# Kernel optimization log

Measured on AMD Instinct MI355X. Metric: run time of the kernel, lower is better.

Reference implementation:

```python
import jax, jax.numpy as jnp
import numpy as np

N_NODES = 50000
N_EDGES = 800000


def gat_layer(x, src, dst, W, al, ar, b, activation):
    # x: [N, F_in], W: [F_in, H*D], al/ar: [H, D], b: [H*D]
    H, D = al.shape
    n = x.shape[0]
    h = (x @ W).reshape(n, H, D)                      # [N, H, D]
    el = jnp.sum(h * al, axis=-1)                     # [N, H]
    er = jnp.sum(h * ar, axis=-1)                     # [N, H]
    e = jax.nn.leaky_relu(el[src] + er[dst], 0.2)     # [E, H]
    # segment softmax over incoming edges of each dst node
    m = jax.ops.segment_max(e, dst, num_segments=n)   # [N, H]
    ex = jnp.exp(e - m[dst])                          # [E, H]
    s = jax.ops.segment_sum(ex, dst, num_segments=n)  # [N, H]
    a = ex / s[dst]                                   # [E, H]
    msg = h[src] * a[:, :, None]                      # [E, H, D]
    out = jax.ops.segment_sum(msg, dst, num_segments=n) + b.reshape(1, H, D)
    return activation(out) if activation is not None else out


def setup_inputs() -> dict:
    key = jax.random.key(0)
    ks = jax.random.split(key, 12)
    feat = jax.random.normal(ks[0], (N_NODES, 128), dtype=jnp.float32)
    src = jax.random.randint(ks[1], (N_EDGES,), 0, N_NODES)
    dst = jax.random.randint(ks[2], (N_EDGES,), 0, N_NODES)
    sc = 0.1
    return {
        "feat": feat, "src": src, "dst": dst,
        "W1": jax.random.normal(ks[3], (128, 256), jnp.float32) * sc,
        "al1": jax.random.normal(ks[4], (4, 64), jnp.float32) * sc,
        "ar1": jax.random.normal(ks[5], (4, 64), jnp.float32) * sc,
        "b1": jnp.zeros((256,), jnp.float32),
        "W2": jax.random.normal(ks[6], (256, 256), jnp.float32) * sc,
        "al2": jax.random.normal(ks[7], (4, 64), jnp.float32) * sc,
        "ar2": jax.random.normal(ks[8], (4, 64), jnp.float32) * sc,
        "b2": jnp.zeros((256,), jnp.float32),
        "W3": jax.random.normal(ks[9], (256, 8), jnp.float32) * sc,
        "al3": jax.random.normal(ks[10], (1, 8), jnp.float32) * sc,
        "ar3": jax.random.normal(ks[11], (1, 8), jnp.float32) * sc,
        "b3": jnp.zeros((8,), jnp.float32),
    }


def reference(feat, src, dst, W1, al1, ar1, b1, W2, al2, ar2, b2, W3, al3, ar3, b3):
    n = feat.shape[0]
    elu = jax.nn.elu
    h = gat_layer(feat, src, dst, W1, al1, ar1, b1, elu).reshape(n, -1)  # flatten heads
    h = gat_layer(h, src, dst, W2, al2, ar2, b2, elu).reshape(n, -1)
    h = gat_layer(h, src, dst, W3, al3, ar3, b3, None)                   # [N, 1, out]
    return h.mean(axis=1)                                               # head mean -> [N, out]
```

## Files before the change

kernel.cpp:

```cpp
#include <hip/hip_runtime.h>
#include <math.h>


typedef _Float16 half8 __attribute__((ext_vector_type(8)));
typedef _Float16 half4 __attribute__((ext_vector_type(4)));
typedef float    floatx4 __attribute__((ext_vector_type(4)));

#define SLOT_CAP 48

__device__ __forceinline__ float leaky02(float x) { return x > 0.f ? x : 0.2f * x; }

__global__ void build_prep(const int* __restrict__ src, const int* __restrict__ dst,
                           int* __restrict__ cnt, unsigned short* __restrict__ slots,
                           const float* __restrict__ W1, _Float16* __restrict__ W1T,
                           const float* __restrict__ W2, _Float16* __restrict__ W2T,
                           int E, int GE) {
    int b = blockIdx.x;
    if (b < GE) {
        int i = b * 256 + threadIdx.x;
        if (i < E) {
            int d = dst[i];
            int p = atomicAdd(&cnt[d], 1);
            if (p < SLOT_CAP) slots[d * SLOT_CAP + p] = (unsigned short)src[i];
        }
    } else {
        int i = (b - GE) * 256 + threadIdx.x;
        if (i < 128 * 256) {
            int m = i >> 7, k = i & 127;
            W1T[i] = (_Float16)W1[k * 256 + m];
        } else {
            int j = i - 128 * 256;
            if (j < 256 * 256) {
                int m = j >> 8, k = j & 255;
                W2T[j] = (_Float16)W2[k * 256 + m];
            }
        }
    }
}

#define GBM 128
#define GBK 32

template <bool AF32>
__global__ __launch_bounds__(256)
void gemm_mfma(const void* __restrict__ Ap, const _Float16* __restrict__ BT,
               _Float16* __restrict__ C, int N, int K) {
    __shared__ _Float16 As[GBM][GBK + 8];
    __shared__ _Float16 Bs[GBM][GBK + 8];
    int tid  = threadIdx.x;
    int wave = tid >> 6, lane = tid & 63;
    int quad = lane >> 4, l16 = lane & 15;
    int row0 = blockIdx.y * GBM;
    int col0 = blockIdx.x * GBM;

    floatx4 acc[8][2];
    #pragma unroll
    for (int i = 0; i < 8; ++i)
        #pragma unroll
        for (int j = 0; j < 2; ++j)
            #pragma unroll
            for (int e = 0; e < 4; ++e) acc[i][j][e] = 0.f;

    for (int k0 = 0; k0 < K; k0 += GBK) {
        if (AF32) {
            const float* Af = (const float*)Ap;
            #pragma unroll
            for (int it = 0; it < 4; ++it) {
                int s = it * 256 + tid;
                int r = s >> 3, off = (s & 7) * 4;
                float4 v = make_float4(0.f, 0.f, 0.f, 0.f);
                int gr = row0 + r;
                if (gr < N) v = *(const float4*)&Af[(size_t)gr * K + k0 + off];
                half4 hv;
                hv[0] = (_Float16)v.x; hv[1] = (_Float16)v.y;
                hv[2] = (_Float16)v.z; hv[3] = (_Float16)v.w;
                *(half4*)&As[r][off] = hv;
            }
        } else {
            const _Float16* Ah = (const _Float16*)Ap;
            #pragma unroll
            for (int it = 0; it < 2; ++it) {
                int s = it * 256 + tid;
                int r = s >> 2, off = (s & 3) * 8;
                half8 v;
                #pragma unroll
                for (int q = 0; q < 8; ++q) v[q] = (_Float16)0.f;
                int gr = row0 + r;
                if (gr < N) v = *(const half8*)&Ah[(size_t)gr * K + k0 + off];
                *(half8*)&As[r][off] = v;
            }
        }
        #pragma unroll
        for (int it = 0; it < 2; ++it) {
            int s = it * 256 + tid;
            int r = s >> 2, off = (s & 3) * 8;
            half8 w = *(const half8*)&BT[(size_t)(col0 + r) * K + k0 + off];
            *(half8*)&Bs[r][off] = w;
        }
        __syncthreads();
        half8 bfrag[2];
        #pragma unroll
        for (int ct = 0; ct < 2; ++ct)
            bfrag[ct] = *(const half8*)&Bs[wave * 32 + ct * 16 + l16][quad * 8];
        #pragma unroll
        for (int rt = 0; rt < 8; ++rt) {
            half8 afrag = *(const half8*)&As[rt * 16 + l16][quad * 8];
            acc[rt][0] = __builtin_amdgcn_mfma_f32_16x16x32_f16(afrag, bfrag[0], acc[rt][0], 0, 0, 0);
            acc[rt][1] = __builtin_amdgcn_mfma_f32_16x16x32_f16(afrag, bfrag[1], acc[rt][1], 0, 0, 0);
        }
        __syncthreads();
    }
    #pragma unroll
    for (int rt = 0; rt < 8; ++rt) {
        #pragma unroll
        for (int reg = 0; reg < 4; ++reg) {
            int gr = row0 + rt * 16 + quad * 4 + reg;
            if (gr < N) {
                #pragma unroll
                for (int ct = 0; ct < 2; ++ct) {
                    int gc = col0 + wave * 32 + ct * 16 + l16;
                    C[(size_t)gr * 256 + gc] = (_Float16)acc[rt][ct][reg];
                }
            }
        }
    }
}

__global__ __launch_bounds__(256)
void attn_lr(const _Float16* __restrict__ h16, const float* __restrict__ al,
             const float* __restrict__ ar, float* __restrict__ el,
             float* __restrict__ er, int NH) {
    int wid = (blockIdx.x * 256 + threadIdx.x) >> 6;
    int lane = threadIdx.x & 63;
    int r = lane >> 3, c = lane & 7;
    int row = wid * 8 + r;
    if (row >= NH) return;
    int hd = row & 3;
    half8 hv = *(const half8*)&h16[(size_t)row * 64 + c * 8];
    const float* alp = &al[hd * 64 + c * 8];
    const float* arp = &ar[hd * 64 + c * 8];
    float l = 0.f, rr = 0.f;
    #pragma unroll
    for (int q = 0; q < 8; ++q) {
        float v = (float)hv[q];
        l  += v * alp[q];
        rr += v * arp[q];
    }
    l  += __shfl_xor(l, 1);  l  += __shfl_xor(l, 2);  l  += __shfl_xor(l, 4);
    rr += __shfl_xor(rr, 1); rr += __shfl_xor(rr, 2); rr += __shfl_xor(rr, 4);
    if (c == 0) { el[row] = l; er[row] = rr; }
}

__global__ __launch_bounds__(256)
void gat_agg(const _Float16* __restrict__ h16, const float* __restrict__ el,
             const float* __restrict__ er, const int* __restrict__ cnt,
             const unsigned short* __restrict__ slots, const float* __restrict__ bias,
             _Float16* __restrict__ out, int N) {
    __shared__ int   sbuf[8][32];
    __shared__ float wbuf[8][32][4];
    int tid = threadIdx.x;
    int l32 = tid & 31;
    int g = tid >> 5;
    int node = blockIdx.x * 8 + g;
    if (node >= N) return;
    int deg = min(cnt[node], SLOT_CAP);
    int beg = node * SLOT_CAP, end = beg + deg;
    int hd = l32 >> 3;

    float4 ern4 = *(const float4*)&er[node * 4];
    float er0 = ern4.x, er1 = ern4.y, er2 = ern4.z, er3 = ern4.w;

    const _Float16* hb = h16 + l32 * 8;
    float acc[8] = {};

    if (deg <= 32) {
        bool act = l32 < deg;
        int sv = 0;
        float e0 = -INFINITY, e1 = -INFINITY, e2 = -INFINITY, e3 = -INFINITY;
        if (act) {
            sv = slots[beg + l32];
            float4 elv = *(const float4*)&el[sv * 4];
            e0 = leaky02(elv.x + er0);
            e1 = leaky02(elv.y + er1);
            e2 = leaky02(elv.z + er2);
            e3 = leaky02(elv.w + er3);
        }
        float m0 = e0, m1 = e1, m2 = e2, m3 = e3;
        #pragma unroll
        for (int msk = 1; msk < 32; msk <<= 1) {
            m0 = fmaxf(m0, __shfl_xor(m0, msk));
            m1 = fmaxf(m1, __shfl_xor(m1, msk));
            m2 = fmaxf(m2, __shfl_xor(m2, msk));
            m3 = fmaxf(m3, __shfl_xor(m3, msk));
        }
        float x0 = act ? __expf(e0 - m0) : 0.f;
        float x1 = act ? __expf(e1 - m1) : 0.f;
        float x2 = act ? __expf(e2 - m2) : 0.f;
        float x3 = act ? __expf(e3 - m3) : 0.f;
        float s0 = x0, s1 = x1, s2 = x2, s3 = x3;
        #pragma unroll
        for (int msk = 1; msk < 32; msk <<= 1) {
            s0 += __shfl_xor(s0, msk);
            s1 += __shfl_xor(s1, msk);
            s2 += __shfl_xor(s2, msk);
            s3 += __shfl_xor(s3, msk);
        }
        float i0 = s0 > 0.f ? 1.f / s0 : 0.f;
        float i1 = s1 > 0.f ? 1.f / s1 : 0.f;
        float i2 = s2 > 0.f ? 1.f / s2 : 0.f;
        float i3 = s3 > 0.f ? 1.f / s3 : 0.f;
        if (act) {
            sbuf[g][l32] = sv;
            wbuf[g][l32][0] = x0 * i0;
            wbuf[g][l32][1] = x1 * i1;
            wbuf[g][l32][2] = x2 * i2;
            wbuf[g][l32][3] = x3 * i3;
        }
        int t = 0;
        for (; t + 4 <= deg; t += 4) {
            int sa = sbuf[g][t],     sb = sbuf[g][t + 1];
            int sc = sbuf[g][t + 2], sd = sbuf[g][t + 3];
            float wa = wbuf[g][t][hd],     wb = wbuf[g][t + 1][hd];
            float wc = wbuf[g][t + 2][hd], wd = wbuf[g][t + 3][hd];
            half8 va = *(const half8*)&hb[(size_t)sa * 256];
            half8 vb = *(const half8*)&hb[(size_t)sb * 256];
            half8 vc = *(const half8*)&hb[(size_t)sc * 256];
            half8 vd = *(const half8*)&hb[(size_t)sd * 256];
            #pragma unroll
            for (int q = 0; q < 8; ++q)
                acc[q] += wa * (float)va[q] + wb * (float)vb[q]
                        + wc * (float)vc[q] + wd * (float)vd[q];
        }
        for (; t < deg; ++t) {
            int s = sbuf[g][t];
            float w = wbuf[g][t][hd];
            half8 v = *(const half8*)&hb[(size_t)s * 256];
            #pragma unroll
            for (int q = 0; q < 8; ++q) acc[q] += w * (float)v[q];
        }
    } else {
        float m0 = -INFINITY, m1 = -INFINITY, m2 = -INFINITY, m3 = -INFINITY;
        for (int j = beg + l32; j < end; j += 32) {
            int sv = slots[j];
            float4 elv = *(const float4*)&el[sv * 4];
            m0 = fmaxf(m0, leaky02(elv.x + er0));
            m1 = fmaxf(m1, leaky02(elv.y + er1));
            m2 = fmaxf(m2, leaky02(elv.z + er2));
            m3 = fmaxf(m3, leaky02(elv.w + er3));
        }
        #pragma unroll
        for (int msk = 1; msk < 32; msk <<= 1) {
            m0 = fmaxf(m0, __shfl_xor(m0, msk));
            m1 = fmaxf(m1, __shfl_xor(m1, msk));
            m2 = fmaxf(m2, __shfl_xor(m2, msk));
            m3 = fmaxf(m3, __shfl_xor(m3, msk));
        }
        float s0 = 0.f, s1 = 0.f, s2 = 0.f, s3 = 0.f;
        for (int j = beg + l32; j < end; j += 32) {
            int sv = slots[j];
            float4 elv = *(const float4*)&el[sv * 4];
            s0 += __expf(leaky02(elv.x + er0) - m0);
            s1 += __expf(leaky02(elv.y + er1) - m1);
            s2 += __expf(leaky02(elv.z + er2) - m2);
            s3 += __expf(leaky02(elv.w + er3) - m3);
        }
        #pragma unroll
        for (int msk = 1; msk < 32; msk <<= 1) {
            s0 += __shfl_xor(s0, msk);
            s1 += __shfl_xor(s1, msk);
            s2 += __shfl_xor(s2, msk);
            s3 += __shfl_xor(s3, msk);
        }
        float mh  = (hd & 2) ? ((hd & 1) ? m3 : m2) : ((hd & 1) ? m1 : m0);
        float sh_ = (hd & 2) ? ((hd & 1) ? s3 : s2) : ((hd & 1) ? s1 : s0);
        float erh = (hd & 2) ? ((hd & 1) ? er3 : er2) : ((hd & 1) ? er1 : er0);
        float ih  = sh_ > 0.f ? 1.f / sh_ : 0.f;
        int j = beg;
        for (; j + 4 <= end; j += 4) {
            int sa = slots[j], sb = slots[j + 1], sc = slots[j + 2], sd = slots[j + 3];
            float wa = __expf(leaky02(el[sa * 4 + hd] + erh) - mh) * ih;
            float wb = __expf(leaky02(el[sb * 4 + hd] + erh) - mh) * ih;
            float wc = __expf(leaky02(el[sc * 4 + hd] + erh) - mh) * ih;
            float wd = __expf(leaky02(el[sd * 4 + hd] + erh) - mh) * ih;
            half8 va = *(const half8*)&hb[(size_t)sa * 256];
            half8 vb = *(const half8*)&hb[(size_t)sb * 256];
            half8 vc = *(const half8*)&hb[(size_t)sc * 256];
            half8 vd = *(const half8*)&hb[(size_t)sd * 256];
            #pragma unroll
            for (int q = 0; q < 8; ++q)
                acc[q] += wa * (float)va[q] + wb * (float)vb[q]
                        + wc * (float)vc[q] + wd * (float)vd[q];
        }
        for (; j < end; ++j) {
            int sv = slots[j];
            float w = __expf(leaky02(el[sv * 4 + hd] + erh) - mh) * ih;
            half8 v = *(const half8*)&hb[(size_t)sv * 256];
            #pragma unroll
            for (int q = 0; q < 8; ++q) acc[q] += w * (float)v[q];
        }
    }

    half8 o;
    #pragma unroll
    for (int q = 0; q < 8; ++q) {
        float v = acc[q] + bias[l32 * 8 + q];
        v = v > 0.f ? v : (__expf(v) - 1.f);
        o[q] = (_Float16)v;
    }
    *(half8*)&out[(size_t)node * 256 + l32 * 8] = o;
}

__global__ __launch_bounds__(256)
void gemm3_attn(const _Float16* __restrict__ x, const float* __restrict__ W,
                const float* __restrict__ al, const float* __restrict__ ar,
                float* __restrict__ h3, float* __restrict__ el,
                float* __restrict__ er, int N) {
    int tid = threadIdx.x;
    int lane = tid & 63;
    int n = blockIdx.x * 4 + (tid >> 6);
    if (n >= N) return;
    float4 wr[8];
    const float4* Wp = (const float4*)&W[lane * 32];
    #pragma unroll
    for (int i = 0; i < 8; ++i) wr[i] = Wp[i];
    half4 xv = *(const half4*)&x[(size_t)n * 256 + lane * 4];
    float acc[8];
    #pragma unroll
    for (int d = 0; d < 8; ++d) acc[d] = 0.f;
    #pragma unroll
    for (int q = 0; q < 4; ++q) {
        float xq = (float)xv[q];
        float4 w0 = wr[q * 2], w1 = wr[q * 2 + 1];
        acc[0] += xq * w0.x; acc[1] += xq * w0.y;
        acc[2] += xq * w0.z; acc[3] += xq * w0.w;
        acc[4] += xq * w1.x; acc[5] += xq * w1.y;
        acc[6] += xq * w1.z; acc[7] += xq * w1.w;
    }
    #pragma unroll
    for (int d = 0; d < 8; ++d) {
        #pragma unroll
        for (int o = 32; o; o >>= 1) acc[d] += __shfl_down(acc[d], o);
    }
    if (lane == 0) {
        float l = 0.f, r = 0.f;
        #pragma unroll
        for (int d = 0; d < 8; ++d) {
            h3[n * 8 + d] = acc[d];
            l += acc[d] * al[d];
            r += acc[d] * ar[d];
        }
        el[n] = l;
        er[n] = r;
    }
}

__global__ __launch_bounds__(256)
void gat_agg3(const float* __restrict__ h3, const float* __restrict__ el,
              const float* __restrict__ er, const int* __restrict__ cnt,
              const unsigned short* __restrict__ slots, const float* __restrict__ bias,
              float* __restrict__ out, int N) {
    __shared__ int   sbuf3[4][64];
    __shared__ float wbuf3[4][64];
    int tid = threadIdx.x;
    int lane = tid & 63;
    int wv = tid >> 6;
    int n = blockIdx.x * 4 + wv;
    if (n >= N) return;
    int deg = min(cnt[n], SLOT_CAP);
    int beg = n * SLOT_CAP;
    float er_n = er[n];
    int g = lane >> 3, c = lane & 7;
    float acc = 0.f;
    bool act = lane < deg;
    int sv = 0;
    float e = -INFINITY;
    if (act) { sv = slots[beg + lane]; e = leaky02(el[sv] + er_n); }
    float mx = e;
    #pragma unroll
    for (int o = 1; o < 64; o <<= 1) mx = fmaxf(mx, __shfl_xor(mx, o));
    float ex = act ? __expf(e - mx) : 0.f;
    float sm = ex;
    #pragma unroll
    for (int o = 1; o < 64; o <<= 1) sm += __shfl_xor(sm, o);
    float inv = sm > 0.f ? 1.f / sm : 0.f;
    if (act) {
        sbuf3[wv][lane] = sv;
        wbuf3[wv][lane] = ex * inv;
    }
    for (int t = g; t < deg; t += 8) {
        int s = sbuf3[wv][t];
        float w = wbuf3[wv][t];
        acc += h3[s * 8 + c] * w;
    }
    acc += __shfl_xor(acc, 8);
    acc += __shfl_xor(acc, 16);
    acc += __shfl_xor(acc, 32);
    if (lane < 8) out[(size_t)n * 8 + lane] = acc + bias[lane];
}

static inline size_t align_up(size_t x, size_t a) { return (x + a - 1) & ~(a - 1); }

extern "C" void kernel_launch(void* const* d_in, const int* in_sizes, int n_in,
                              void* d_out, int out_size, void* d_ws, size_t ws_size,
                              hipStream_t stream) {
    const float* feat = (const float*)d_in[0];
    const int*   src  = (const int*)d_in[1];
    const int*   dst  = (const int*)d_in[2];
    const float* W1   = (const float*)d_in[3];
    const float* al1  = (const float*)d_in[4];
    const float* ar1  = (const float*)d_in[5];
    const float* b1   = (const float*)d_in[6];
    const float* W2   = (const float*)d_in[7];
    const float* al2  = (const float*)d_in[8];
    const float* ar2  = (const float*)d_in[9];
    const float* b2   = (const float*)d_in[10];
    const float* W3   = (const float*)d_in[11];
    const float* al3  = (const float*)d_in[12];
    const float* ar3  = (const float*)d_in[13];
    const float* b3   = (const float*)d_in[14];

    const int N = in_sizes[0] / 128;
    const int E = in_sizes[1];

    char* w = (char*)d_ws;
    _Float16* bufA16 = (_Float16*)w; w += align_up((size_t)N * 256 * 2, 256);
    _Float16* bufB16 = (_Float16*)w; w += align_up((size_t)N * 256 * 2, 256);
    _Float16* W1T    = (_Float16*)w; w += align_up((size_t)256 * 128 * 2, 256);
    _Float16* W2T    = (_Float16*)w; w += align_up((size_t)256 * 256 * 2, 256);
    float* el      = (float*)w; w += align_up((size_t)N * 4 * 4, 256);
    float* er      = (float*)w; w += align_up((size_t)N * 4 * 4, 256);
    int*   cnt     = (int*)w;   w += align_up((size_t)N * 4, 256);
    unsigned short* slots = (unsigned short*)w;
    w += align_up((size_t)N * SLOT_CAP * 2, 256);
    float* h3 = (float*)bufA16;
    (void)ws_size; (void)n_in; (void)out_size;

    const int GE = (E + 255) / 256;
    const int GT = (128 * 256 + 256 * 256 + 255) / 256;

    hipMemsetAsync(cnt, 0, (size_t)N * 4, stream);
    build_prep<<<GE + GT, 256, 0, stream>>>(src, dst, cnt, slots,
                                            W1, W1T, W2, W2T, E, GE);

    dim3 ggrid(2, (N + GBM - 1) / GBM);
    const int GA = (N + 7) / 8;
    const int GL = (N * 4 + 31) / 32;

    gemm_mfma<true><<<ggrid, 256, 0, stream>>>(feat, W1T, bufA16, N, 128);
    attn_lr<<<GL, 256, 0, stream>>>(bufA16, al1, ar1, el, er, N * 4);
    gat_agg<<<GA, 256, 0, stream>>>(bufA16, el, er, cnt, slots, b1, bufB16, N);

    gemm_mfma<false><<<ggrid, 256, 0, stream>>>(bufB16, W2T, bufA16, N, 256);
    attn_lr<<<GL, 256, 0, stream>>>(bufA16, al2, ar2, el, er, N * 4);
    gat_agg<<<GA, 256, 0, stream>>>(bufA16, el, er, cnt, slots, b2, bufB16, N);

    gemm3_attn<<<(N + 3) / 4, 256, 0, stream>>>(bufB16, W3, al3, ar3, h3, el, er, N);
    gat_agg3<<<(N + 3) / 4, 256, 0, stream>>>(h3, el, er, cnt, slots, b3,
                                              (float*)d_out, N);
}
```

Before: 390.8 us.

## Fuse all GAT stages into one persistent kernel with grid-wide barriers

Replaces the eight separate kernel launches with a single persistent kernel of 960 blocks. The blocks loop over virtual block indices for each stage and separate the stages with an atomic-counter grid barrier. The aim is to remove launch gaps and per-kernel tail effects. In exchange it depends on all 960 blocks being co-resident (four per CU is requested), otherwise the barrier deadlocks or hits its spin timeout. The barrier itself adds fence and spin cost, and the shared-memory footprint is now the GEMM's maximum for every stage.

```diff
diff --git a/kernel.cpp b/kernel.cpp
--- a/kernel.cpp
+++ b/kernel.cpp
@@ -7,51 +7,36 @@
 typedef float    floatx4 __attribute__((ext_vector_type(4)));
 
 #define SLOT_CAP 48
-
-__device__ __forceinline__ float leaky02(float x) { return x > 0.f ? x : 0.2f * x; }
-
-__global__ void build_prep(const int* __restrict__ src, const int* __restrict__ dst,
-                           int* __restrict__ cnt, unsigned short* __restrict__ slots,
-                           const float* __restrict__ W1, _Float16* __restrict__ W1T,
-                           const float* __restrict__ W2, _Float16* __restrict__ W2T,
-                           int E, int GE) {
-    int b = blockIdx.x;
-    if (b < GE) {
-        int i = b * 256 + threadIdx.x;
-        if (i < E) {
-            int d = dst[i];
-            int p = atomicAdd(&cnt[d], 1);
-            if (p < SLOT_CAP) slots[d * SLOT_CAP + p] = (unsigned short)src[i];
-        }
-    } else {
-        int i = (b - GE) * 256 + threadIdx.x;
-        if (i < 128 * 256) {
-            int m = i >> 7, k = i & 127;
-            W1T[i] = (_Float16)W1[k * 256 + m];
-        } else {
-            int j = i - 128 * 256;
-            if (j < 256 * 256) {
-                int m = j >> 8, k = j & 255;
-                W2T[j] = (_Float16)W2[k * 256 + m];
-            }
-        }
-    }
-}
-
 #define GBM 128
 #define GBK 32
+#define NBLK 960
+
+__device__ __forceinline__ float leaky02(float x) { return x > 0.f ? x : 0.2f * x; }
+
+__device__ __forceinline__ void gsync(int* bar, int target) {
+    __syncthreads();
+    if (threadIdx.x == 0) {
+        __threadfence();
+        atomicAdd(bar, 1);
+        int spins = 0;
+        while (__hip_atomic_load(bar, __ATOMIC_RELAXED, __HIP_MEMORY_SCOPE_AGENT) < target) {
+            if (++spins > (1 << 30)) break;
+        }
+        __threadfence();
+    }
+    __syncthreads();
+}
 
 template <bool AF32>
-__global__ __launch_bounds__(256)
-void gemm_mfma(const void* __restrict__ Ap, const _Float16* __restrict__ BT,
-               _Float16* __restrict__ C, int N, int K) {
-    __shared__ _Float16 As[GBM][GBK + 8];
-    __shared__ _Float16 Bs[GBM][GBK + 8];
+__device__ __forceinline__ void gemm_tile(char* smem, const void* __restrict__ Ap,
+                                          const _Float16* __restrict__ BT,
+                                          _Float16* __restrict__ C,
+                                          int row0, int col0, int N, int K) {
+    _Float16 (*As)[GBK + 8] = (_Float16 (*)[GBK + 8])smem;
+    _Float16 (*Bs)[GBK + 8] = (_Float16 (*)[GBK + 8])(smem + GBM * (GBK + 8) * 2);
     int tid  = threadIdx.x;
     int wave = tid >> 6, lane = tid & 63;
     int quad = lane >> 4, l16 = lane & 15;
-    int row0 = blockIdx.y * GBM;
-    int col0 = blockIdx.x * GBM;
 
     floatx4 acc[8][2];
     #pragma unroll
@@ -126,12 +111,13 @@
     }
 }
 
-__global__ __launch_bounds__(256)
-void attn_lr(const _Float16* __restrict__ h16, const float* __restrict__ al,
-             const float* __restrict__ ar, float* __restrict__ el,
-             float* __restrict__ er, int NH) {
-    int wid = (blockIdx.x * 256 + threadIdx.x) >> 6;
+__device__ __forceinline__ void attn_body(int vb, const _Float16* __restrict__ h16,
+                                          const float* __restrict__ al,
+                                          const float* __restrict__ ar,
+                                          float* __restrict__ el, float* __restrict__ er,
+                                          int NH) {
     int lane = threadIdx.x & 63;
+    int wid = vb * 4 + (threadIdx.x >> 6);
     int r = lane >> 3, c = lane & 7;
     int row = wid * 8 + r;
     if (row >= NH) return;
@@ -151,17 +137,20 @@
     if (c == 0) { el[row] = l; er[row] = rr; }
 }
 
-__global__ __launch_bounds__(256)
-void gat_agg(const _Float16* __restrict__ h16, const float* __restrict__ el,
-             const float* __restrict__ er, const int* __restrict__ cnt,
-             const unsigned short* __restrict__ slots, const float* __restrict__ bias,
-             _Float16* __restrict__ out, int N) {
-    __shared__ int   sbuf[8][32];
-    __shared__ float wbuf[8][32][4];
+__device__ __forceinline__ void agg_body(int vb, char* smem,
+                                         const _Float16* __restrict__ h16,
+                                         const float* __restrict__ el,
+                                         const float* __restrict__ er,
+                                         const int* __restrict__ cnt,
+                                         const unsigned short* __restrict__ slots,
+                                         const float* __restrict__ bias,
+                                         _Float16* __restrict__ out, int N) {
+    int (*sbuf)[32]     = (int (*)[32])smem;
+    float (*wbuf)[32][4] = (float (*)[32][4])(smem + 1024);
     int tid = threadIdx.x;
     int l32 = tid & 31;
     int g = tid >> 5;
-    int node = blockIdx.x * 8 + g;
+    int node = vb * 8 + g;
     if (node >= N) return;
     int deg = min(cnt[node], SLOT_CAP);
     int beg = node * SLOT_CAP, end = beg + deg;
@@ -223,12 +212,12 @@
             float wa = wbuf[g][t][hd],     wb = wbuf[g][t + 1][hd];
             float wc = wbuf[g][t + 2][hd], wd = wbuf[g][t + 3][hd];
             half8 va = *(const half8*)&hb[(size_t)sa * 256];
-            half8 vb = *(const half8*)&hb[(size_t)sb * 256];
+            half8 vb2 = *(const half8*)&hb[(size_t)sb * 256];
             half8 vc = *(const half8*)&hb[(size_t)sc * 256];
             half8 vd = *(const half8*)&hb[(size_t)sd * 256];
             #pragma unroll
             for (int q = 0; q < 8; ++q)
-                acc[q] += wa * (float)va[q] + wb * (float)vb[q]
+                acc[q] += wa * (float)va[q] + wb * (float)vb2[q]
                         + wc * (float)vc[q] + wd * (float)vd[q];
         }
         for (; t < deg; ++t) {
@@ -283,12 +272,12 @@
             float wc = __expf(leaky02(el[sc * 4 + hd] + erh) - mh) * ih;
             float wd = __expf(leaky02(el[sd * 4 + hd] + erh) - mh) * ih;
             half8 va = *(const half8*)&hb[(size_t)sa * 256];
-            half8 vb = *(const half8*)&hb[(size_t)sb * 256];
+            half8 vb2 = *(const half8*)&hb[(size_t)sb * 256];
             half8 vc = *(const half8*)&hb[(size_t)sc * 256];
             half8 vd = *(const half8*)&hb[(size_t)sd * 256];
             #pragma unroll
             for (int q = 0; q < 8; ++q)
-                acc[q] += wa * (float)va[q] + wb * (float)vb[q]
+                acc[q] += wa * (float)va[q] + wb * (float)vb2[q]
                         + wc * (float)vc[q] + wd * (float)vd[q];
         }
         for (; j < end; ++j) {
@@ -310,92 +299,165 @@
     *(half8*)&out[(size_t)node * 256 + l32 * 8] = o;
 }
 
-__global__ __launch_bounds__(256)
-void gemm3_attn(const _Float16* __restrict__ x, const float* __restrict__ W,
-                const float* __restrict__ al, const float* __restrict__ ar,
-                float* __restrict__ h3, float* __restrict__ el,
-                float* __restrict__ er, int N) {
-    int tid = threadIdx.x;
-    int lane = tid & 63;
-    int n = blockIdx.x * 4 + (tid >> 6);
-    if (n >= N) return;
-    float4 wr[8];
-    const float4* Wp = (const float4*)&W[lane * 32];
-    #pragma unroll
-    for (int i = 0; i < 8; ++i) wr[i] = Wp[i];
-    half4 xv = *(const half4*)&x[(size_t)n * 256 + lane * 4];
-    float acc[8];
-    #pragma unroll
-    for (int d = 0; d < 8; ++d) acc[d] = 0.f;
-    #pragma unroll
-    for (int q = 0; q < 4; ++q) {
-        float xq = (float)xv[q];
-        float4 w0 = wr[q * 2], w1 = wr[q * 2 + 1];
-        acc[0] += xq * w0.x; acc[1] += xq * w0.y;
-        acc[2] += xq * w0.z; acc[3] += xq * w0.w;
-        acc[4] += xq * w1.x; acc[5] += xq * w1.y;
-        acc[6] += xq * w1.z; acc[7] += xq * w1.w;
-    }
-    #pragma unroll
-    for (int d = 0; d < 8; ++d) {
-        #pragma unroll
-        for (int o = 32; o; o >>= 1) acc[d] += __shfl_down(acc[d], o);
-    }
-    if (lane == 0) {
-        float l = 0.f, r = 0.f;
-        #pragma unroll
-        for (int d = 0; d < 8; ++d) {
-            h3[n * 8 + d] = acc[d];
-            l += acc[d] * al[d];
-            r += acc[d] * ar[d];
-        }
-        el[n] = l;
-        er[n] = r;
-    }
-}
-
-__global__ __launch_bounds__(256)
-void gat_agg3(const float* __restrict__ h3, const float* __restrict__ el,
-              const float* __restrict__ er, const int* __restrict__ cnt,
-              const unsigned short* __restrict__ slots, const float* __restrict__ bias,
-              float* __restrict__ out, int N) {
-    __shared__ int   sbuf3[4][64];
-    __shared__ float wbuf3[4][64];
-    int tid = threadIdx.x;
-    int lane = tid & 63;
-    int wv = tid >> 6;
-    int n = blockIdx.x * 4 + wv;
-    if (n >= N) return;
-    int deg = min(cnt[n], SLOT_CAP);
-    int beg = n * SLOT_CAP;
-    float er_n = er[n];
-    int g = lane >> 3, c = lane & 7;
-    float acc = 0.f;
-    bool act = lane < deg;
-    int sv = 0;
-    float e = -INFINITY;
-    if (act) { sv = slots[beg + lane]; e = leaky02(el[sv] + er_n); }
-    float mx = e;
-    #pragma unroll
-    for (int o = 1; o < 64; o <<= 1) mx = fmaxf(mx, __shfl_xor(mx, o));
-    float ex = act ? __expf(e - mx) : 0.f;
-    float sm = ex;
-    #pragma unroll
-    for (int o = 1; o < 64; o <<= 1) sm += __shfl_xor(sm, o);
-    float inv = sm > 0.f ? 1.f / sm : 0.f;
-    if (act) {
-        sbuf3[wv][lane] = sv;
-        wbuf3[wv][lane] = ex * inv;
-    }
-    for (int t = g; t < deg; t += 8) {
-        int s = sbuf3[wv][t];
-        float w = wbuf3[wv][t];
-        acc += h3[s * 8 + c] * w;
-    }
-    acc += __shfl_xor(acc, 8);
-    acc += __shfl_xor(acc, 16);
-    acc += __shfl_xor(acc, 32);
-    if (lane < 8) out[(size_t)n * 8 + lane] = acc + bias[lane];
+__global__ __launch_bounds__(256, 4)
+void gat_fused(const float* __restrict__ feat, const int* __restrict__ src,
+               const int* __restrict__ dst,
+               const float* __restrict__ W1, const float* __restrict__ al1,
+               const float* __restrict__ ar1, const float* __restrict__ b1,
+               const float* __restrict__ W2, const float* __restrict__ al2,
+               const float* __restrict__ ar2, const float* __restrict__ b2,
+               const float* __restrict__ W3, const float* __restrict__ al3,
+               const float* __restrict__ ar3, const float* __restrict__ b3,
+               _Float16* bufA16, _Float16* bufB16,
+               _Float16* W1T, _Float16* W2T,
+               float* el, float* er, int* cnt, unsigned short* slots,
+               int* bar, float* outp, int N, int E) {
+    __shared__ __align__(16) char smem[2 * GBM * (GBK + 8) * 2];
+    const int G = gridDim.x;
+    const int tid = threadIdx.x;
+    int sync_no = 0;
+
+    {
+        int GE = (E + 255) / 256;
+        int GT = (128 * 256 + 256 * 256 + 255) / 256;
+        for (int vb = blockIdx.x; vb < GE + GT; vb += G) {
+            if (vb < GE) {
+                int i = vb * 256 + tid;
+                if (i < E) {
+                    int d = dst[i];
+                    int p = atomicAdd(&cnt[d], 1);
+                    if (p < SLOT_CAP) slots[d * SLOT_CAP + p] = (unsigned short)src[i];
+                }
+            } else {
+                int i = (vb - GE) * 256 + tid;
+                if (i < 128 * 256) {
+                    int m = i >> 7, k = i & 127;
+                    W1T[i] = (_Float16)W1[k * 256 + m];
+                } else {
+                    int j = i - 128 * 256;
+                    if (j < 256 * 256) {
+                        int m = j >> 8, k = j & 255;
+                        W2T[j] = (_Float16)W2[k * 256 + m];
+                    }
+                }
+            }
+        }
+    }
+    gsync(bar, ++sync_no * G);
+
+    int TILES = (N + GBM - 1) / GBM;
+    int VB_ATT = (N * 4 + 31) / 32;
+    int VB_AGG = (N + 7) / 8;
+    int VB_W4  = (N + 3) / 4;
+
+    for (int vb = blockIdx.x; vb < 2 * TILES; vb += G)
+        gemm_tile<true>(smem, feat, W1T, bufA16, (vb >> 1) * GBM, (vb & 1) * GBM, N, 128);
+    gsync(bar, ++sync_no * G);
+
+    for (int vb = blockIdx.x; vb < VB_ATT; vb += G)
+        attn_body(vb, bufA16, al1, ar1, el, er, N * 4);
+    gsync(bar, ++sync_no * G);
+
+    for (int vb = blockIdx.x; vb < VB_AGG; vb += G)
+        agg_body(vb, smem, bufA16, el, er, cnt, slots, b1, bufB16, N);
+    gsync(bar, ++sync_no * G);
+
+    for (int vb = blockIdx.x; vb < 2 * TILES; vb += G)
+        gemm_tile<false>(smem, bufB16, W2T, bufA16, (vb >> 1) * GBM, (vb & 1) * GBM, N, 256);
+    gsync(bar, ++sync_no * G);
+
+    for (int vb = blockIdx.x; vb < VB_ATT; vb += G)
+        attn_body(vb, bufA16, al2, ar2, el, er, N * 4);
+    gsync(bar, ++sync_no * G);
+
+    for (int vb = blockIdx.x; vb < VB_AGG; vb += G)
+        agg_body(vb, smem, bufA16, el, er, cnt, slots, b2, bufB16, N);
+    gsync(bar, ++sync_no * G);
+
+    {
+        float* h3 = (float*)bufA16;
+        int lane = tid & 63;
+        for (int vb = blockIdx.x; vb < VB_W4; vb += G) {
+            int n = vb * 4 + (tid >> 6);
+            if (n >= N) continue;
+            float4 wr[8];
+            const float4* Wp = (const float4*)&W3[lane * 32];
+            #pragma unroll
+            for (int i = 0; i < 8; ++i) wr[i] = Wp[i];
+            half4 xv = *(const half4*)&bufB16[(size_t)n * 256 + lane * 4];
+            float acc[8];
+            #pragma unroll
+            for (int d = 0; d < 8; ++d) acc[d] = 0.f;
+            #pragma unroll
+            for (int q = 0; q < 4; ++q) {
+                float xq = (float)xv[q];
+                float4 w0 = wr[q * 2], w1 = wr[q * 2 + 1];
+                acc[0] += xq * w0.x; acc[1] += xq * w0.y;
+                acc[2] += xq * w0.z; acc[3] += xq * w0.w;
+                acc[4] += xq * w1.x; acc[5] += xq * w1.y;
+                acc[6] += xq * w1.z; acc[7] += xq * w1.w;
+            }
+            #pragma unroll
+            for (int d = 0; d < 8; ++d) {
+                #pragma unroll
+                for (int o = 32; o; o >>= 1) acc[d] += __shfl_down(acc[d], o);
+            }
+            if (lane == 0) {
+                float l = 0.f, r = 0.f;
+                #pragma unroll
+                for (int d = 0; d < 8; ++d) {
+                    h3[n * 8 + d] = acc[d];
+                    l += acc[d] * al3[d];
+                    r += acc[d] * ar3[d];
+                }
+                el[n] = l;
+                er[n] = r;
+            }
+        }
+    }
+    gsync(bar, ++sync_no * G);
+
+    {
+        const float* h3 = (const float*)bufA16;
+        int (*sbuf3)[64]  = (int (*)[64])smem;
+        float (*wbuf3)[64] = (float (*)[64])(smem + 1024);
+        int lane = tid & 63;
+        int wv = tid >> 6;
+        int g = lane >> 3, c = lane & 7;
+        for (int vb = blockIdx.x; vb < VB_W4; vb += G) {
+            int n = vb * 4 + wv;
+            if (n >= N) continue;
+            int deg = min(cnt[n], SLOT_CAP);
+            int beg = n * SLOT_CAP;
+            float er_n = er[n];
+            float acc = 0.f;
+            bool act = lane < deg;
+            int sv = 0;
+            float e = -INFINITY;
+            if (act) { sv = slots[beg + lane]; e = leaky02(el[sv] + er_n); }
+            float mx = e;
+            #pragma unroll
+            for (int o = 1; o < 64; o <<= 1) mx = fmaxf(mx, __shfl_xor(mx, o));
+            float ex = act ? __expf(e - mx) : 0.f;
+            float sm = ex;
+            #pragma unroll
+            for (int o = 1; o < 64; o <<= 1) sm += __shfl_xor(sm, o);
+            float inv = sm > 0.f ? 1.f / sm : 0.f;
+            if (act) {
+                sbuf3[wv][lane] = sv;
+                wbuf3[wv][lane] = ex * inv;
+            }
+            for (int t = g; t < deg; t += 8) {
+                int s = sbuf3[wv][t];
+                float w = wbuf3[wv][t];
+                acc += h3[s * 8 + c] * w;
+            }
+            acc += __shfl_xor(acc, 8);
+            acc += __shfl_xor(acc, 16);
+            acc += __shfl_xor(acc, 32);
+            if (lane < 8) outp[(size_t)n * 8 + lane] = acc + b3[lane];
+        }
+    }
 }
 
 static inline size_t align_up(size_t x, size_t a) { return (x + a - 1) & ~(a - 1); }
@@ -429,32 +491,19 @@
     _Float16* W2T    = (_Float16*)w; w += align_up((size_t)256 * 256 * 2, 256);
     float* el      = (float*)w; w += align_up((size_t)N * 4 * 4, 256);
     float* er      = (float*)w; w += align_up((size_t)N * 4 * 4, 256);
+    int*   bar     = (int*)w;   w += 256;
     int*   cnt     = (int*)w;   w += align_up((size_t)N * 4, 256);
     unsigned short* slots = (unsigned short*)w;
     w += align_up((size_t)N * SLOT_CAP * 2, 256);
-    float* h3 = (float*)bufA16;
     (void)ws_size; (void)n_in; (void)out_size;
 
-    const int GE = (E + 255) / 256;
-    const int GT = (128 * 256 + 256 * 256 + 255) / 256;
-
-    hipMemsetAsync(cnt, 0, (size_t)N * 4, stream);
-    build_prep<<<GE + GT, 256, 0, stream>>>(src, dst, cnt, slots,
-                                            W1, W1T, W2, W2T, E, GE);
-
-    dim3 ggrid(2, (N + GBM - 1) / GBM);
-    const int GA = (N + 7) / 8;
-    const int GL = (N * 4 + 31) / 32;
-
-    gemm_mfma<true><<<ggrid, 256, 0, stream>>>(feat, W1T, bufA16, N, 128);
-    attn_lr<<<GL, 256, 0, stream>>>(bufA16, al1, ar1, el, er, N * 4);
-    gat_agg<<<GA, 256, 0, stream>>>(bufA16, el, er, cnt, slots, b1, bufB16, N);
-
-    gemm_mfma<false><<<ggrid, 256, 0, stream>>>(bufB16, W2T, bufA16, N, 256);
-    attn_lr<<<GL, 256, 0, stream>>>(bufA16, al2, ar2, el, er, N * 4);
-    gat_agg<<<GA, 256, 0, stream>>>(bufA16, el, er, cnt, slots, b2, bufB16, N);
-
-    gemm3_attn<<<(N + 3) / 4, 256, 0, stream>>>(bufB16, W3, al3, ar3, h3, el, er, N);
-    gat_agg3<<<(N + 3) / 4, 256, 0, stream>>>(h3, el, er, cnt, slots, b3,
-                                              (float*)d_out, N);
+    (void)hipMemsetAsync(bar, 0, 256 + align_up((size_t)N * 4, 256), stream);
+
+    gat_fused<<<NBLK, 256, 0, stream>>>(feat, src, dst,
+                                        W1, al1, ar1, b1,
+                                        W2, al2, ar2, b2,
+                                        W3, al3, ar3, b3,
+                                        bufA16, bufB16, W1T, W2T,
+                                        el, er, cnt, slots, bar,
+                                        (float*)d_out, N, E);
 }
```

After: 1.451 ms. +271.3%, slower.
